# Performance work log

Hardware: AMD Instinct MI355X
Metric: run time of the kernel (lower is better)

Reference implementation:

```python
import jax, jax.numpy as jnp
import numpy as np

B = 8192
N = 2048  # output_dim; input_dim = 4*N


def setup_inputs() -> dict:
    key = jax.random.key(0)
    k1, k2, k3, k4, k5 = jax.random.split(key, 5)
    weight = jax.random.normal(k1, (B, 4 * N), dtype=jnp.float32)
    fc_w = jax.random.normal(k2, (N, 4 * N), dtype=jnp.float32) * 0.02
    fc_b = jax.random.normal(k3, (N,), dtype=jnp.float32) * 0.02
    # per-sample coin flips (torch.rand(1) < 0.5), precomputed as constants
    swap1 = jax.random.randint(k4, (B,), 0, 2, dtype=jnp.int32)
    swap2 = jax.random.randint(k5, (B,), 0, 2, dtype=jnp.int32)
    return {"weight": weight, "fc_w": fc_w, "fc_b": fc_b, "swap1": swap1, "swap2": swap2}


def _permute_rows(x, swap1, swap2):
    # x: [B, 4, n]. Sequential swaps: first swap rows (1,2) if swap1, then
    # swap rows (2,3) (of the already-swapped tensor) if swap2.
    s1 = swap1.astype(bool)
    s2 = swap2.astype(bool)
    r0 = jnp.zeros_like(swap1)
    r1 = jnp.where(s1, 2, 1)
    mid = jnp.where(s1, 1, 2)  # what sits at row 2 after swap1
    r2 = jnp.where(s2, 3, mid)
    r3 = jnp.where(s2, mid, 3)
    perm = jnp.stack([r0, r1, r2, r3], axis=1)  # [B, 4]
    return jnp.take_along_axis(x, perm[:, :, None], axis=1)


def reference(weight, fc_w, fc_b, swap1, swap2):
    b = weight.shape[0]
    n = fc_w.shape[0]
    x = weight.reshape(b, 4, n)
    x = _permute_rows(x, swap1, swap2)
    x = x.reshape(b, 4 * n)
    return x @ fc_w.T + fc_b
```

## Files before the change

kernel.cpp:

```cpp
#include <hip/hip_runtime.h>
#include <hip/hip_bf16.h>
#include <stdint.h>


using f32x4   = __attribute__((ext_vector_type(4))) float;
using bf16x8  = __attribute__((ext_vector_type(8))) __bf16;
using ushort8 = __attribute__((ext_vector_type(8))) unsigned short;

#define B_ROWS 8192
#define K_TOT  8192
#define N_OUT  2048
#define BK     64
#define NT     (K_TOT / BK)

__device__ __forceinline__ unsigned short f2bf(float f) {
  union { float f; unsigned int u; } v;
  v.f = f;
  unsigned int r = v.u + 0x7FFFu + ((v.u >> 16) & 1u);
  return (unsigned short)(r >> 16);
}

__device__ __forceinline__ int perm_src(int r, int s1, int s2) {
  int mid = s1 ? 1 : 2;
  return (r == 0) ? 0
       : (r == 1) ? (s1 ? 2 : 1)
       : (r == 2) ? (s2 ? 3 : mid)
                  : (s2 ? mid : 3);
}

__global__ __launch_bounds__(256) void k_permute_convert(
    const float* __restrict__ w, const int* __restrict__ s1v,
    const int* __restrict__ s2v, unsigned short* __restrict__ xbf) {
  const int blk = blockIdx.x;
  const int b = blk >> 2, r = blk & 3;
  const int s1 = s1v[b] != 0, s2 = s2v[b] != 0;
  const int pr = perm_src(r, s1, s2);
  const float* src = w + (size_t)b * K_TOT + (size_t)pr * 2048 + threadIdx.x * 8;
  unsigned short* dst = xbf + (size_t)b * K_TOT + (size_t)r * 2048 + threadIdx.x * 8;
  f32x4 v0 = *(const f32x4*)src;
  f32x4 v1 = *(const f32x4*)(src + 4);
  ushort8 o;
#pragma unroll
  for (int j = 0; j < 4; ++j) o[j] = f2bf(v0[j]);
#pragma unroll
  for (int j = 0; j < 4; ++j) o[4 + j] = f2bf(v1[j]);
  *(ushort8*)dst = o;
}

__global__ __launch_bounds__(256) void k_convert_w(
    const float* __restrict__ fw, unsigned short* __restrict__ wbf) {
  const size_t base = ((size_t)blockIdx.x * 256 + threadIdx.x) * 8;
  f32x4 v0 = *(const f32x4*)(fw + base);
  f32x4 v1 = *(const f32x4*)(fw + base + 4);
  ushort8 o;
#pragma unroll
  for (int j = 0; j < 4; ++j) o[j] = f2bf(v0[j]);
#pragma unroll
  for (int j = 0; j < 4; ++j) o[4 + j] = f2bf(v1[j]);
  *(ushort8*)(wbf + base) = o;
}

__device__ __forceinline__ void gload16(const unsigned short* g,
                                        const unsigned short* l) {
  __builtin_amdgcn_global_load_lds(
      (__attribute__((address_space(1))) void*)(uintptr_t)(const void*)g,
      (__attribute__((address_space(3))) void*)(unsigned int)(uintptr_t)(const void*)l,
      16, 0, 0);
}


#define VMW4 asm volatile("s_waitcnt vmcnt(4)" ::: "memory")
#define VMW0 asm volatile("s_waitcnt vmcnt(0)" ::: "memory")
#define VMWN ((void)0)
#define LGKM0_FENCE do { \
    asm volatile("s_waitcnt lgkmcnt(0)" ::: "memory"); \
    __builtin_amdgcn_sched_barrier(0); } while (0)

#define LDA(BU, MH, M, KKI) \
  (*(const bf16x8*)(smb + (BU)*65536 + aBase + ((MH)*64 + (M)*16)*128 + colsw[KKI]))
#define LDB(BU, NH, N, KKI) \
  (*(const bf16x8*)(smb + (BU)*65536 + 32768 + bBase + ((NH)*32 + (N)*16)*128 + colsw[KKI]))

#define STAGE(BU, OPL, GOP, H, T) do { \
  gload16((GOP) + (size_t)((H)*128 + row0) * K_TOT + (size_t)(T)*BK + sl0, \
          smu + (BU)*32768 + (OPL) + (H)*8192 + tid*8); \
  gload16((GOP) + (size_t)((H)*128 + row1) * K_TOT + (size_t)(T)*BK + sl1, \
          smu + (BU)*32768 + (OPL) + (H)*8192 + 4096 + tid*8); \
} while (0)

#define QUAD(MH, NH, B0A, B1A) do { \
  _Pragma("unroll") for (int m_ = 0; m_ < 4; ++m_) \
    _Pragma("unroll") for (int n_ = 0; n_ < 2; ++n_) { \
      acc[(MH)*4+m_][(NH)*2+n_] = __builtin_amdgcn_mfma_f32_16x16x32_bf16( \
          aR0[m_], B0A[n_], acc[(MH)*4+m_][(NH)*2+n_], 0, 0, 0); \
      acc[(MH)*4+m_][(NH)*2+n_] = __builtin_amdgcn_mfma_f32_16x16x32_bf16( \
          aR1[m_], B1A[n_], acc[(MH)*4+m_][(NH)*2+n_], 0, 0, 0); \
    } \
} while (0)

#define TILE(BU, T, DOA, DOB, WAIT) do { \
  _Pragma("unroll") for (int m_ = 0; m_ < 4; ++m_) { \
    aR0[m_] = LDA(BU, 0, m_, 0); aR1[m_] = LDA(BU, 0, m_, 1); } \
  _Pragma("unroll") for (int n_ = 0; n_ < 2; ++n_) { \
    bL0[n_] = LDB(BU, 0, n_, 0); bL1[n_] = LDB(BU, 0, n_, 1); } \
  if (DOA) STAGE((BU) ^ 1, 0, gA, 0, (T) + 1); \
  __builtin_amdgcn_s_barrier(); \
  LGKM0_FENCE; \
  __builtin_amdgcn_s_setprio(1); QUAD(0, 0, bL0, bL1); __builtin_amdgcn_s_setprio(0); \
  __builtin_amdgcn_s_barrier(); \
  _Pragma("unroll") for (int n_ = 0; n_ < 2; ++n_) { \
    bH0[n_] = LDB(BU, 1, n_, 0); bH1[n_] = LDB(BU, 1, n_, 1); } \
  if (DOA) STAGE((BU) ^ 1, 0, gA, 1, (T) + 1); \
  __builtin_amdgcn_s_barrier(); \
  LGKM0_FENCE; \
  __builtin_amdgcn_s_setprio(1); QUAD(0, 1, bH0, bH1); __builtin_amdgcn_s_setprio(0); \
  __builtin_amdgcn_s_barrier(); \
  _Pragma("unroll") for (int m_ = 0; m_ < 4; ++m_) { \
    aR0[m_] = LDA(BU, 1, m_, 0); aR1[m_] = LDA(BU, 1, m_, 1); } \
  if (DOB) STAGE(BU, 16384, gB, 0, (T) + 2); \
  __builtin_amdgcn_s_barrier(); \
  LGKM0_FENCE; \
  __builtin_amdgcn_s_setprio(1); QUAD(1, 0, bL0, bL1); __builtin_amdgcn_s_setprio(0); \
  __builtin_amdgcn_s_barrier(); \
  if (DOB) STAGE(BU, 16384, gB, 1, (T) + 2); \
  __builtin_amdgcn_s_barrier(); \
  __builtin_amdgcn_s_setprio(1); QUAD(1, 1, bH0, bH1); __builtin_amdgcn_s_setprio(0); \
  WAIT; \
  __builtin_amdgcn_s_barrier(); \
} while (0)

__global__ __launch_bounds__(512, 2) void k_gemm8(
    const unsigned short* __restrict__ A,
    const unsigned short* __restrict__ Bw,
    const float* __restrict__ bias,
    float* __restrict__ C) {
  __shared__ unsigned short sm[2 * 32768];
  unsigned short* smu = sm;
  const char* smb = (const char*)sm;

  const int tid  = threadIdx.x;
  const int lane = tid & 63;
  const int wave = tid >> 6;
  const int wr = wave >> 2;
  const int wc = wave & 3;
  const int bn = blockIdx.x & 7;
  const int bm = blockIdx.x >> 3;

  const unsigned short* gA = A  + (size_t)bm * 256 * K_TOT;
  const unsigned short* gB = Bw + (size_t)bn * 256 * K_TOT;

  const int row0 = tid >> 3;
  const int sl0  = (((tid & 7) ^ (row0 & 7)) << 3);
  const int row1 = (512 + tid) >> 3;
  const int sl1  = ((((512 + tid) & 7) ^ (row1 & 7)) << 3);

  const int l15 = lane & 15;
  int colsw[2];
  colsw[0] = (((lane >> 4) << 4)) ^ ((lane & 7) << 4);
  colsw[1] = (64 | ((lane >> 4) << 4)) ^ ((lane & 7) << 4);
  const int aBase = (wr * 128 + l15) * 128;
  const int bBase = (wc * 64 + l15) * 128;

  f32x4 acc[8][4];
#pragma unroll
  for (int i = 0; i < 8; ++i)
#pragma unroll
    for (int j = 0; j < 4; ++j) {
      acc[i][j][0] = 0.f; acc[i][j][1] = 0.f; acc[i][j][2] = 0.f; acc[i][j][3] = 0.f;
    }
  bf16x8 aR0[4], aR1[4], bL0[2], bL1[2], bH0[2], bH1[2];

  STAGE(0, 0,     gA, 0, 0);
  STAGE(0, 0,     gA, 1, 0);
  STAGE(0, 16384, gB, 0, 0);
  STAGE(0, 16384, gB, 1, 0);
  STAGE(1, 16384, gB, 0, 1);
  STAGE(1, 16384, gB, 1, 1);
  VMW4;
  __builtin_amdgcn_s_barrier();

  int t = 0;
  for (; t < NT - 4; t += 2) {
    TILE(0, t,     true, true, VMW4);
    TILE(1, t + 1, true, true, VMW4);
  }
  TILE(0, 124, true,  true,  VMW4);
  TILE(1, 125, true,  true,  VMW4);
  TILE(0, 126, true,  false, VMW0);
  TILE(1, 127, false, false, VMWN);

  const int crow0 = bm * 256 + wr * 128 + ((lane >> 4) << 2);
  const int ccol0 = bn * 256 + wc * 64 + l15;
  float bv[4];
#pragma unroll
  for (int n = 0; n < 4; ++n) bv[n] = bias[ccol0 + n * 16];
#pragma unroll
  for (int mi = 0; mi < 8; ++mi)
#pragma unroll
    for (int ni = 0; ni < 4; ++ni) {
      const int r = crow0 + mi * 16;
      const int c = ccol0 + ni * 16;
#pragma unroll
      for (int j = 0; j < 4; ++j)
        C[(size_t)(r + j) * N_OUT + c] = acc[mi][ni][j] + bv[ni];
    }
}

__global__ __launch_bounds__(256) void k_gemm_fallback(
    const float* __restrict__ W, const float* __restrict__ FW,
    const float* __restrict__ bias, const int* __restrict__ s1v,
    const int* __restrict__ s2v, float* __restrict__ C) {
  __shared__ float As[64][33];
  __shared__ float Bs[64][33];
  const int tid = threadIdx.x;
  const int tx = tid & 15, ty = tid >> 4;
  const int bm = blockIdx.x & 127;
  const int bn = blockIdx.x >> 7;
  float acc[4][4] = {{0.f}};
  for (int k0 = 0; k0 < K_TOT; k0 += 32) {
#pragma unroll
    for (int i = 0; i < 8; ++i) {
      int idx = i * 256 + tid;
      int rr = idx >> 5, cc = idx & 31;
      int grow = bm * 64 + rr;
      int gk = k0 + cc;
      int blkr = gk >> 11, within = gk & 2047;
      int s1 = s1v[grow] != 0, s2 = s2v[grow] != 0;
      int pr = perm_src(blkr, s1, s2);
      As[rr][cc] = W[(size_t)grow * K_TOT + (size_t)pr * 2048 + within];
      Bs[rr][cc] = FW[(size_t)(bn * 64 + rr) * K_TOT + gk];
    }
    __syncthreads();
#pragma unroll 8
    for (int kk = 0; kk < 32; ++kk) {
      float a[4], b[4];
#pragma unroll
      for (int i = 0; i < 4; ++i) a[i] = As[ty * 4 + i][kk];
#pragma unroll
      for (int j = 0; j < 4; ++j) b[j] = Bs[tx * 4 + j][kk];
#pragma unroll
      for (int i = 0; i < 4; ++i)
#pragma unroll
        for (int j = 0; j < 4; ++j) acc[i][j] += a[i] * b[j];
    }
    __syncthreads();
  }
#pragma unroll
  for (int i = 0; i < 4; ++i)
#pragma unroll
    for (int j = 0; j < 4; ++j) {
      int r = bm * 64 + ty * 4 + i, c = bn * 64 + tx * 4 + j;
      C[(size_t)r * N_OUT + c] = acc[i][j] + bias[c];
    }
}

extern "C" void kernel_launch(void* const* d_in, const int* in_sizes, int n_in,
                              void* d_out, int out_size, void* d_ws, size_t ws_size,
                              hipStream_t stream) {
  const float* weight = (const float*)d_in[0];
  const float* fc_w   = (const float*)d_in[1];
  const float* fc_b   = (const float*)d_in[2];
  const int*   swap1  = (const int*)d_in[3];
  const int*   swap2  = (const int*)d_in[4];
  float* out = (float*)d_out;

  const size_t xbf_bytes = (size_t)B_ROWS * K_TOT * 2;
  const size_t wbf_bytes = (size_t)N_OUT * K_TOT * 2;
  if (ws_size >= xbf_bytes + wbf_bytes) {
    unsigned short* xbf = (unsigned short*)d_ws;
    unsigned short* wbf = (unsigned short*)((char*)d_ws + xbf_bytes);
    k_permute_convert<<<B_ROWS * 4, 256, 0, stream>>>(weight, swap1, swap2, xbf);
    k_convert_w<<<(N_OUT * K_TOT) / 2048, 256, 0, stream>>>(fc_w, wbf);
    k_gemm8<<<32 * 8, 512, 0, stream>>>(xbf, wbf, fc_b, out);
  } else {
    k_gemm_fallback<<<128 * 32, 256, 0, stream>>>(weight, fc_w, fc_b, swap1,
                                                  swap2, out);
  }
}
```

Measured before the change: 295.7 us.

## Load B operand directly from global into registers and merge prep kernels

The GEMM now keeps only the A tile in LDS and loads the B (weight) fragments straight from global memory into registers, prefetching the next k-step. This halves the shared-memory footprint and drops most barriers per tile. The two fp32-to-bf16 prep kernels are merged into one launch to save a launch and a tail. The cost is that B reads bypass LDS reuse: each wave fetches its own B fragments from global/L2 with less coalesced access, and every tile now ends with a full vmcnt(0) wait.

Result: slower. 474.0 us (+60.3%).

```diff
diff --git a/kernel.cpp b/kernel.cpp
--- a/kernel.cpp
+++ b/kernel.cpp
@@ -28,15 +28,24 @@
                   : (s2 ? mid : 3);
 }
 
-__global__ __launch_bounds__(256) void k_permute_convert(
+__global__ __launch_bounds__(256) void k_prep(
     const float* __restrict__ w, const int* __restrict__ s1v,
-    const int* __restrict__ s2v, unsigned short* __restrict__ xbf) {
+    const int* __restrict__ s2v, const float* __restrict__ fw,
+    unsigned short* __restrict__ xbf, unsigned short* __restrict__ wbf) {
   const int blk = blockIdx.x;
-  const int b = blk >> 2, r = blk & 3;
-  const int s1 = s1v[b] != 0, s2 = s2v[b] != 0;
-  const int pr = perm_src(r, s1, s2);
-  const float* src = w + (size_t)b * K_TOT + (size_t)pr * 2048 + threadIdx.x * 8;
-  unsigned short* dst = xbf + (size_t)b * K_TOT + (size_t)r * 2048 + threadIdx.x * 8;
+  const float* src;
+  unsigned short* dst;
+  if (blk < B_ROWS * 4) {
+    const int b = blk >> 2, r = blk & 3;
+    const int s1 = s1v[b] != 0, s2 = s2v[b] != 0;
+    const int pr = perm_src(r, s1, s2);
+    src = w + (size_t)b * K_TOT + (size_t)pr * 2048 + threadIdx.x * 8;
+    dst = xbf + (size_t)b * K_TOT + (size_t)r * 2048 + threadIdx.x * 8;
+  } else {
+    const size_t base = ((size_t)(blk - B_ROWS * 4) * 256 + threadIdx.x) * 8;
+    src = fw + base;
+    dst = wbf + base;
+  }
   f32x4 v0 = *(const f32x4*)src;
   f32x4 v1 = *(const f32x4*)(src + 4);
   ushort8 o;
@@ -45,19 +54,6 @@
 #pragma unroll
   for (int j = 0; j < 4; ++j) o[4 + j] = f2bf(v1[j]);
   *(ushort8*)dst = o;
-}
-
-__global__ __launch_bounds__(256) void k_convert_w(
-    const float* __restrict__ fw, unsigned short* __restrict__ wbf) {
-  const size_t base = ((size_t)blockIdx.x * 256 + threadIdx.x) * 8;
-  f32x4 v0 = *(const f32x4*)(fw + base);
-  f32x4 v1 = *(const f32x4*)(fw + base + 4);
-  ushort8 o;
-#pragma unroll
-  for (int j = 0; j < 4; ++j) o[j] = f2bf(v0[j]);
-#pragma unroll
-  for (int j = 0; j < 4; ++j) o[4 + j] = f2bf(v1[j]);
-  *(ushort8*)(wbf + base) = o;
 }
 
 __device__ __forceinline__ void gload16(const unsigned short* g,
@@ -68,73 +64,53 @@
       16, 0, 0);
 }
 
-
-#define VMW4 asm volatile("s_waitcnt vmcnt(4)" ::: "memory")
 #define VMW0 asm volatile("s_waitcnt vmcnt(0)" ::: "memory")
-#define VMWN ((void)0)
 #define LGKM0_FENCE do { \
     asm volatile("s_waitcnt lgkmcnt(0)" ::: "memory"); \
     __builtin_amdgcn_sched_barrier(0); } while (0)
 
-#define LDA(BU, MH, M, KKI) \
-  (*(const bf16x8*)(smb + (BU)*65536 + aBase + ((MH)*64 + (M)*16)*128 + colsw[KKI]))
-#define LDB(BU, NH, N, KKI) \
-  (*(const bf16x8*)(smb + (BU)*65536 + 32768 + bBase + ((NH)*32 + (N)*16)*128 + colsw[KKI]))
-
-#define STAGE(BU, OPL, GOP, H, T) do { \
-  gload16((GOP) + (size_t)((H)*128 + row0) * K_TOT + (size_t)(T)*BK + sl0, \
-          smu + (BU)*32768 + (OPL) + (H)*8192 + tid*8); \
-  gload16((GOP) + (size_t)((H)*128 + row1) * K_TOT + (size_t)(T)*BK + sl1, \
-          smu + (BU)*32768 + (OPL) + (H)*8192 + 4096 + tid*8); \
-} while (0)
-
-#define QUAD(MH, NH, B0A, B1A) do { \
-  _Pragma("unroll") for (int m_ = 0; m_ < 4; ++m_) \
-    _Pragma("unroll") for (int n_ = 0; n_ < 2; ++n_) { \
-      acc[(MH)*4+m_][(NH)*2+n_] = __builtin_amdgcn_mfma_f32_16x16x32_bf16( \
-          aR0[m_], B0A[n_], acc[(MH)*4+m_][(NH)*2+n_], 0, 0, 0); \
-      acc[(MH)*4+m_][(NH)*2+n_] = __builtin_amdgcn_mfma_f32_16x16x32_bf16( \
-          aR1[m_], B1A[n_], acc[(MH)*4+m_][(NH)*2+n_], 0, 0, 0); \
-    } \
-} while (0)
-
-#define TILE(BU, T, DOA, DOB, WAIT) do { \
-  _Pragma("unroll") for (int m_ = 0; m_ < 4; ++m_) { \
-    aR0[m_] = LDA(BU, 0, m_, 0); aR1[m_] = LDA(BU, 0, m_, 1); } \
-  _Pragma("unroll") for (int n_ = 0; n_ < 2; ++n_) { \
-    bL0[n_] = LDB(BU, 0, n_, 0); bL1[n_] = LDB(BU, 0, n_, 1); } \
-  if (DOA) STAGE((BU) ^ 1, 0, gA, 0, (T) + 1); \
+#define ALD(BUF, KK) do { \
+  _Pragma("unroll") for (int m_ = 0; m_ < 8; ++m_) \
+    ar[m_] = *(const bf16x8*)(smb + (BUF)*32768 + m_*2048 + aCol[KK]); \
+} while (0)
+
+#define BLD(DST, T, KKH) do { \
+  _Pragma("unroll") for (int n_ = 0; n_ < 4; ++n_) \
+    DST[n_] = *(const bf16x8*)(gBb + (boff0 + n_*262144 + (KKH)*64 + (unsigned)(T)*128)); \
+} while (0)
+
+#define APF(BUF, T) do { \
+  _Pragma("unroll") for (int r_ = 0; r_ < 4; ++r_) \
+    gload16(pa0 + (size_t)r_*524288 + (size_t)(T)*64, \
+            smu + (BUF)*16384 + r_*4096 + tid*8); \
+} while (0)
+
+#define MM(BSET) do { \
+  _Pragma("unroll") for (int m_ = 0; m_ < 8; ++m_) \
+    _Pragma("unroll") for (int n_ = 0; n_ < 4; ++n_) \
+      acc[m_][n_] = __builtin_amdgcn_mfma_f32_16x16x32_bf16( \
+          ar[m_], BSET[n_], acc[m_][n_], 0, 0, 0); \
+} while (0)
+
+#define TILE(BUF, T, BK0C, BK0P, DOPF) do { \
+  ALD(BUF, 0); \
+  BLD(bk1, T, 1);                     \
+  if (DOPF) { BLD(BK0P, (T) + 1, 0); APF((BUF) ^ 1, (T) + 1); } \
+  LGKM0_FENCE; \
+  __builtin_amdgcn_s_setprio(1); MM(BK0C); __builtin_amdgcn_s_setprio(0); \
+  ALD(BUF, 1); \
+  LGKM0_FENCE; \
+  __builtin_amdgcn_s_setprio(1); MM(bk1); __builtin_amdgcn_s_setprio(0); \
+  VMW0; \
   __builtin_amdgcn_s_barrier(); \
-  LGKM0_FENCE; \
-  __builtin_amdgcn_s_setprio(1); QUAD(0, 0, bL0, bL1); __builtin_amdgcn_s_setprio(0); \
-  __builtin_amdgcn_s_barrier(); \
-  _Pragma("unroll") for (int n_ = 0; n_ < 2; ++n_) { \
-    bH0[n_] = LDB(BU, 1, n_, 0); bH1[n_] = LDB(BU, 1, n_, 1); } \
-  if (DOA) STAGE((BU) ^ 1, 0, gA, 1, (T) + 1); \
-  __builtin_amdgcn_s_barrier(); \
-  LGKM0_FENCE; \
-  __builtin_amdgcn_s_setprio(1); QUAD(0, 1, bH0, bH1); __builtin_amdgcn_s_setprio(0); \
-  __builtin_amdgcn_s_barrier(); \
-  _Pragma("unroll") for (int m_ = 0; m_ < 4; ++m_) { \
-    aR0[m_] = LDA(BU, 1, m_, 0); aR1[m_] = LDA(BU, 1, m_, 1); } \
-  if (DOB) STAGE(BU, 16384, gB, 0, (T) + 2); \
-  __builtin_amdgcn_s_barrier(); \
-  LGKM0_FENCE; \
-  __builtin_amdgcn_s_setprio(1); QUAD(1, 0, bL0, bL1); __builtin_amdgcn_s_setprio(0); \
-  __builtin_amdgcn_s_barrier(); \
-  if (DOB) STAGE(BU, 16384, gB, 1, (T) + 2); \
-  __builtin_amdgcn_s_barrier(); \
-  __builtin_amdgcn_s_setprio(1); QUAD(1, 1, bH0, bH1); __builtin_amdgcn_s_setprio(0); \
-  WAIT; \
-  __builtin_amdgcn_s_barrier(); \
-} while (0)
-
-__global__ __launch_bounds__(512, 2) void k_gemm8(
+} while (0)
+
+__global__ __launch_bounds__(512, 2) void k_gemm9(
     const unsigned short* __restrict__ A,
     const unsigned short* __restrict__ Bw,
     const float* __restrict__ bias,
     float* __restrict__ C) {
-  __shared__ unsigned short sm[2 * 32768];
+  __shared__ unsigned short sm[2 * 16384];
   unsigned short* smu = sm;
   const char* smb = (const char*)sm;
 
@@ -145,21 +121,23 @@
   const int wc = wave & 3;
   const int bn = blockIdx.x & 7;
   const int bm = blockIdx.x >> 3;
-
-  const unsigned short* gA = A  + (size_t)bm * 256 * K_TOT;
-  const unsigned short* gB = Bw + (size_t)bn * 256 * K_TOT;
-
-  const int row0 = tid >> 3;
-  const int sl0  = (((tid & 7) ^ (row0 & 7)) << 3);
-  const int row1 = (512 + tid) >> 3;
-  const int sl1  = ((((512 + tid) & 7) ^ (row1 & 7)) << 3);
-
   const int l15 = lane & 15;
-  int colsw[2];
-  colsw[0] = (((lane >> 4) << 4)) ^ ((lane & 7) << 4);
-  colsw[1] = (64 | ((lane >> 4) << 4)) ^ ((lane & 7) << 4);
-  const int aBase = (wr * 128 + l15) * 128;
-  const int bBase = (wc * 64 + l15) * 128;
+
+  const unsigned short* gA = A + (size_t)bm * 256 * K_TOT;
+  const char* gBb = (const char*)(Bw + (size_t)bn * 256 * K_TOT);
+
+  const unsigned short* pa0 =
+      gA + (size_t)(tid >> 3) * K_TOT + (size_t)(((tid & 7) ^ ((tid >> 3) & 7)) * 8);
+
+  int aCol[2];
+  {
+    const int rowb = (wr * 128 + l15) * 128;
+    aCol[0] = rowb + ((((lane >> 4) << 4)) ^ ((lane & 7) << 4));
+    aCol[1] = rowb + ((64 | ((lane >> 4) << 4)) ^ ((lane & 7) << 4));
+  }
+
+  const unsigned int boff0 =
+      (unsigned int)((wc * 64 + l15) * (K_TOT * 2) + ((lane >> 4) << 4));
 
   f32x4 acc[8][4];
 #pragma unroll
@@ -168,26 +146,21 @@
     for (int j = 0; j < 4; ++j) {
       acc[i][j][0] = 0.f; acc[i][j][1] = 0.f; acc[i][j][2] = 0.f; acc[i][j][3] = 0.f;
     }
-  bf16x8 aR0[4], aR1[4], bL0[2], bL1[2], bH0[2], bH1[2];
-
-  STAGE(0, 0,     gA, 0, 0);
-  STAGE(0, 0,     gA, 1, 0);
-  STAGE(0, 16384, gB, 0, 0);
-  STAGE(0, 16384, gB, 1, 0);
-  STAGE(1, 16384, gB, 0, 1);
-  STAGE(1, 16384, gB, 1, 1);
-  VMW4;
+  bf16x8 ar[8], bk0a[4], bk0b[4], bk1[4];
+
+  APF(0, 0);
+  BLD(bk0a, 0, 0);
+  VMW0;
   __builtin_amdgcn_s_barrier();
 
-  int t = 0;
-  for (; t < NT - 4; t += 2) {
-    TILE(0, t,     true, true, VMW4);
-    TILE(1, t + 1, true, true, VMW4);
-  }
-  TILE(0, 124, true,  true,  VMW4);
-  TILE(1, 125, true,  true,  VMW4);
-  TILE(0, 126, true,  false, VMW0);
-  TILE(1, 127, false, false, VMWN);
+  for (int t = 0; t < NT - 4; t += 2) {
+    TILE(0, t,     bk0a, bk0b, true);
+    TILE(1, t + 1, bk0b, bk0a, true);
+  }
+  TILE(0, 124, bk0a, bk0b, true);
+  TILE(1, 125, bk0b, bk0a, true);
+  TILE(0, 126, bk0a, bk0b, true);
+  TILE(1, 127, bk0b, bk0a, false);
 
   const int crow0 = bm * 256 + wr * 128 + ((lane >> 4) << 2);
   const int ccol0 = bn * 256 + wc * 64 + l15;
@@ -269,9 +242,9 @@
   if (ws_size >= xbf_bytes + wbf_bytes) {
     unsigned short* xbf = (unsigned short*)d_ws;
     unsigned short* wbf = (unsigned short*)((char*)d_ws + xbf_bytes);
-    k_permute_convert<<<B_ROWS * 4, 256, 0, stream>>>(weight, swap1, swap2, xbf);
-    k_convert_w<<<(N_OUT * K_TOT) / 2048, 256, 0, stream>>>(fc_w, wbf);
-    k_gemm8<<<32 * 8, 512, 0, stream>>>(xbf, wbf, fc_b, out);
+    k_prep<<<B_ROWS * 4 + (N_OUT * K_TOT) / 2048, 256, 0, stream>>>(
+        weight, swap1, swap2, fc_w, xbf, wbf);
+    k_gemm9<<<32 * 8, 512, 0, stream>>>(xbf, wbf, fc_b, out);
   } else {
     k_gemm_fallback<<<128 * 32, 256, 0, stream>>>(weight, fc_w, fc_b, swap1,
                                                   swap2, out);
```

## Fuse row permutation and bf16 conversion of activations into the GEMM A-loader

Applied to the files above, without the earlier changes.

Removes the separate permute/convert kernel and its bf16 activation workspace. The GEMM now reads fp32 activation rows directly through register loads. Each row's source chunk is picked from packed permutation bits, and the values are converted to bf16 and written into swizzled LDS. Only the weight matrix is still pre-converted and streamed with direct-to-LDS loads. This saves a full read and write pass over the activations. In exchange, the GEMM reads fp32 A, twice as many bytes, once per N-tile, and adds register pressure plus VALU conversion work inside the main loop.

After: 381.5 us. 1.29x slower.

```diff
diff --git a/kernel.cpp b/kernel.cpp
--- a/kernel.cpp
+++ b/kernel.cpp
@@ -18,6 +18,14 @@
   v.f = f;
   unsigned int r = v.u + 0x7FFFu + ((v.u >> 16) & 1u);
   return (unsigned short)(r >> 16);
+}
+
+__device__ __forceinline__ int perm_pack(int s1, int s2) {
+  int mid = s1 ? 1 : 2;
+  int r1 = s1 ? 2 : 1;
+  int r2 = s2 ? 3 : mid;
+  int r3 = s2 ? mid : 3;
+  return (r1 << 2) | (r2 << 4) | (r3 << 6);
 }
 
 __device__ __forceinline__ int perm_src(int r, int s1, int s2) {
@@ -28,26 +36,7 @@
                   : (s2 ? mid : 3);
 }
 
-__global__ __launch_bounds__(256) void k_permute_convert(
-    const float* __restrict__ w, const int* __restrict__ s1v,
-    const int* __restrict__ s2v, unsigned short* __restrict__ xbf) {
-  const int blk = blockIdx.x;
-  const int b = blk >> 2, r = blk & 3;
-  const int s1 = s1v[b] != 0, s2 = s2v[b] != 0;
-  const int pr = perm_src(r, s1, s2);
-  const float* src = w + (size_t)b * K_TOT + (size_t)pr * 2048 + threadIdx.x * 8;
-  unsigned short* dst = xbf + (size_t)b * K_TOT + (size_t)r * 2048 + threadIdx.x * 8;
-  f32x4 v0 = *(const f32x4*)src;
-  f32x4 v1 = *(const f32x4*)(src + 4);
-  ushort8 o;
-#pragma unroll
-  for (int j = 0; j < 4; ++j) o[j] = f2bf(v0[j]);
-#pragma unroll
-  for (int j = 0; j < 4; ++j) o[4 + j] = f2bf(v1[j]);
-  *(ushort8*)dst = o;
-}
-
-__global__ __launch_bounds__(256) void k_convert_w(
+__global__ __launch_bounds__(256) void k_prep_w(
     const float* __restrict__ fw, unsigned short* __restrict__ wbf) {
   const size_t base = ((size_t)blockIdx.x * 256 + threadIdx.x) * 8;
   f32x4 v0 = *(const f32x4*)(fw + base);
@@ -68,10 +57,9 @@
       16, 0, 0);
 }
 
-
-#define VMW4 asm volatile("s_waitcnt vmcnt(4)" ::: "memory")
-#define VMW0 asm volatile("s_waitcnt vmcnt(0)" ::: "memory")
-#define VMWN ((void)0)
+#define VM0 asm volatile("s_waitcnt vmcnt(0)" ::: "memory")
+#define VM2 asm volatile("s_waitcnt vmcnt(2)" ::: "memory")
+#define NOW ((void)0)
 #define LGKM0_FENCE do { \
     asm volatile("s_waitcnt lgkmcnt(0)" ::: "memory"); \
     __builtin_amdgcn_sched_barrier(0); } while (0)
@@ -81,11 +69,34 @@
 #define LDB(BU, NH, N, KKI) \
   (*(const bf16x8*)(smb + (BU)*65536 + 32768 + bBase + ((NH)*32 + (N)*16)*128 + colsw[KKI]))
 
-#define STAGE(BU, OPL, GOP, H, T) do { \
-  gload16((GOP) + (size_t)((H)*128 + row0) * K_TOT + (size_t)(T)*BK + sl0, \
-          smu + (BU)*32768 + (OPL) + (H)*8192 + tid*8); \
-  gload16((GOP) + (size_t)((H)*128 + row1) * K_TOT + (size_t)(T)*BK + sl1, \
-          smu + (BU)*32768 + (OPL) + (H)*8192 + 4096 + tid*8); \
+#define ALD(BUF, MH) do { \
+  _Pragma("unroll") for (int m_ = 0; m_ < 4; ++m_) { \
+    aR0[m_] = LDA(BUF, MH, m_, 0); aR1[m_] = LDA(BUF, MH, m_, 1); } \
+} while (0)
+
+#define STAGEB(BUF, H, T) do { \
+  gload16(gB + (size_t)((H)*128 + row0) * K_TOT + (size_t)(T)*BK + sl0, \
+          smu + (BUF)*32768 + 16384 + (H)*8192 + tid*8); \
+  gload16(gB + (size_t)((H)*128 + row1) * K_TOT + (size_t)(T)*BK + sl0, \
+          smu + (BUF)*32768 + 16384 + (H)*8192 + 4096 + tid*8); \
+} while (0)
+
+#define AOFF(PK, TK) \
+  ((size_t)((((PK) >> ((((TK) >> 5)) << 1)) & 3) << 11) + (size_t)(((TK) & 31) << 6))
+#define ARL0(TK) do { const float* p_ = pA0 + AOFF(PA0, TK); \
+  a0f[0] = *(const f32x4*)p_;        a0f[1] = *(const f32x4*)(p_ + 4); \
+  a0f[2] = *(const f32x4*)(p_ + 8);  a0f[3] = *(const f32x4*)(p_ + 12); } while (0)
+#define ARL1(TK) do { const float* p_ = pA1 + AOFF(PA1, TK); \
+  a1f[0] = *(const f32x4*)p_;        a1f[1] = *(const f32x4*)(p_ + 4); \
+  a1f[2] = *(const f32x4*)(p_ + 8);  a1f[3] = *(const f32x4*)(p_ + 12); } while (0)
+
+#define AWR(BUF, H, AF) do { \
+  bf16x8 lo_, hi_; \
+  _Pragma("unroll") for (int j_ = 0; j_ < 4; ++j_) { \
+    lo_[j_]     = (__bf16)AF[0][j_]; lo_[4 + j_] = (__bf16)AF[1][j_]; \
+    hi_[j_]     = (__bf16)AF[2][j_]; hi_[4 + j_] = (__bf16)AF[3][j_]; } \
+  char* d_ = smw + (BUF)*65536 + ((H)*128 + arow) * 128; \
+  *(bf16x8*)(d_ + wb0) = lo_; *(bf16x8*)(d_ + wb1) = hi_; \
 } while (0)
 
 #define QUAD(MH, NH, B0A, B1A) do { \
@@ -98,45 +109,48 @@
     } \
 } while (0)
 
-#define TILE(BU, T, DOA, DOB, WAIT) do { \
-  _Pragma("unroll") for (int m_ = 0; m_ < 4; ++m_) { \
-    aR0[m_] = LDA(BU, 0, m_, 0); aR1[m_] = LDA(BU, 0, m_, 1); } \
+#define TILE_F(BUF, T, DOA, DOB, WA0, WA1) do { \
+  ALD(BUF, 0); \
   _Pragma("unroll") for (int n_ = 0; n_ < 2; ++n_) { \
-    bL0[n_] = LDB(BU, 0, n_, 0); bL1[n_] = LDB(BU, 0, n_, 1); } \
-  if (DOA) STAGE((BU) ^ 1, 0, gA, 0, (T) + 1); \
+    bL0[n_] = LDB(BUF, 0, n_, 0); bL1[n_] = LDB(BUF, 0, n_, 1); } \
+  if (DOA) ARL0((T) + 1); \
   __builtin_amdgcn_s_barrier(); \
   LGKM0_FENCE; \
   __builtin_amdgcn_s_setprio(1); QUAD(0, 0, bL0, bL1); __builtin_amdgcn_s_setprio(0); \
   __builtin_amdgcn_s_barrier(); \
   _Pragma("unroll") for (int n_ = 0; n_ < 2; ++n_) { \
-    bH0[n_] = LDB(BU, 1, n_, 0); bH1[n_] = LDB(BU, 1, n_, 1); } \
-  if (DOA) STAGE((BU) ^ 1, 0, gA, 1, (T) + 1); \
+    bH0[n_] = LDB(BUF, 1, n_, 0); bH1[n_] = LDB(BUF, 1, n_, 1); } \
   __builtin_amdgcn_s_barrier(); \
   LGKM0_FENCE; \
   __builtin_amdgcn_s_setprio(1); QUAD(0, 1, bH0, bH1); __builtin_amdgcn_s_setprio(0); \
   __builtin_amdgcn_s_barrier(); \
-  _Pragma("unroll") for (int m_ = 0; m_ < 4; ++m_) { \
-    aR0[m_] = LDA(BU, 1, m_, 0); aR1[m_] = LDA(BU, 1, m_, 1); } \
-  if (DOB) STAGE(BU, 16384, gB, 0, (T) + 2); \
+  ALD(BUF, 1); \
+  if (DOB) STAGEB(BUF, 0, (T) + 2); \
+  WA0; \
+  if (DOA) { AWR((BUF) ^ 1, 0, a0f); ARL1((T) + 1); } \
   __builtin_amdgcn_s_barrier(); \
   LGKM0_FENCE; \
   __builtin_amdgcn_s_setprio(1); QUAD(1, 0, bL0, bL1); __builtin_amdgcn_s_setprio(0); \
   __builtin_amdgcn_s_barrier(); \
-  if (DOB) STAGE(BU, 16384, gB, 1, (T) + 2); \
+  if (DOB) STAGEB(BUF, 1, (T) + 2); \
+  WA1; \
+  if (DOA) AWR((BUF) ^ 1, 1, a1f); \
   __builtin_amdgcn_s_barrier(); \
   __builtin_amdgcn_s_setprio(1); QUAD(1, 1, bH0, bH1); __builtin_amdgcn_s_setprio(0); \
-  WAIT; \
-  __builtin_amdgcn_s_barrier(); \
-} while (0)
-
-__global__ __launch_bounds__(512, 2) void k_gemm8(
-    const unsigned short* __restrict__ A,
+  asm volatile("s_waitcnt lgkmcnt(0)" ::: "memory"); \
+  __builtin_amdgcn_s_barrier(); \
+} while (0)
+
+__global__ __launch_bounds__(512, 2) void k_gemm10(
+    const float* __restrict__ W,
+    const int* __restrict__ s1v, const int* __restrict__ s2v,
     const unsigned short* __restrict__ Bw,
     const float* __restrict__ bias,
     float* __restrict__ C) {
   __shared__ unsigned short sm[2 * 32768];
   unsigned short* smu = sm;
   const char* smb = (const char*)sm;
+  char* smw = (char*)sm;
 
   const int tid  = threadIdx.x;
   const int lane = tid & 63;
@@ -145,16 +159,25 @@
   const int wc = wave & 3;
   const int bn = blockIdx.x & 7;
   const int bm = blockIdx.x >> 3;
-
-  const unsigned short* gA = A  + (size_t)bm * 256 * K_TOT;
+  const int l15 = lane & 15;
+
   const unsigned short* gB = Bw + (size_t)bn * 256 * K_TOT;
 
   const int row0 = tid >> 3;
+  const int row1 = 64 + row0;
   const int sl0  = (((tid & 7) ^ (row0 & 7)) << 3);
-  const int row1 = (512 + tid) >> 3;
-  const int sl1  = ((((512 + tid) & 7) ^ (row1 & 7)) << 3);
-
-  const int l15 = lane & 15;
+
+  const int arow = tid >> 2;
+  const int c16  = (tid & 3) << 4;
+  const int rA0 = bm * 256 + arow;
+  const int rA1 = rA0 + 128;
+  const float* pA0 = W + (size_t)rA0 * K_TOT + c16;
+  const float* pA1 = W + (size_t)rA1 * K_TOT + c16;
+  const int PA0 = perm_pack(s1v[rA0] != 0, s2v[rA0] != 0);
+  const int PA1 = perm_pack(s1v[rA1] != 0, s2v[rA1] != 0);
+  const int wb0 = ((((tid & 3) * 2)    ) ^ (arow & 7)) << 4;
+  const int wb1 = ((((tid & 3) * 2) | 1) ^ (arow & 7)) << 4;
+
   int colsw[2];
   colsw[0] = (((lane >> 4) << 4)) ^ ((lane & 7) << 4);
   colsw[1] = (64 | ((lane >> 4) << 4)) ^ ((lane & 7) << 4);
@@ -169,25 +192,24 @@
       acc[i][j][0] = 0.f; acc[i][j][1] = 0.f; acc[i][j][2] = 0.f; acc[i][j][3] = 0.f;
     }
   bf16x8 aR0[4], aR1[4], bL0[2], bL1[2], bH0[2], bH1[2];
-
-  STAGE(0, 0,     gA, 0, 0);
-  STAGE(0, 0,     gA, 1, 0);
-  STAGE(0, 16384, gB, 0, 0);
-  STAGE(0, 16384, gB, 1, 0);
-  STAGE(1, 16384, gB, 0, 1);
-  STAGE(1, 16384, gB, 1, 1);
-  VMW4;
+  f32x4 a0f[4], a1f[4];
+
+  STAGEB(0, 0, 0); STAGEB(0, 1, 0);
+  STAGEB(1, 0, 1); STAGEB(1, 1, 1);
+  ARL0(0); ARL1(0);
+  VM0;
+  AWR(0, 0, a0f); AWR(0, 1, a1f);
+  LGKM0_FENCE;
   __builtin_amdgcn_s_barrier();
 
-  int t = 0;
-  for (; t < NT - 4; t += 2) {
-    TILE(0, t,     true, true, VMW4);
-    TILE(1, t + 1, true, true, VMW4);
+  for (int t = 0; t < 124; t += 2) {
+    TILE_F(0, t,     true, true, VM2, VM2);
+    TILE_F(1, t + 1, true, true, VM2, VM2);
   }
-  TILE(0, 124, true,  true,  VMW4);
-  TILE(1, 125, true,  true,  VMW4);
-  TILE(0, 126, true,  false, VMW0);
-  TILE(1, 127, false, false, VMWN);
+  TILE_F(0, 124, true,  true,  VM2, VM2);
+  TILE_F(1, 125, true,  true,  VM2, VM2);
+  TILE_F(0, 126, true,  false, VM0, VM0);
+  TILE_F(1, 127, false, false, NOW, NOW);
 
   const int crow0 = bm * 256 + wr * 128 + ((lane >> 4) << 2);
   const int ccol0 = bn * 256 + wc * 64 + l15;
@@ -264,14 +286,11 @@
   const int*   swap2  = (const int*)d_in[4];
   float* out = (float*)d_out;
 
-  const size_t xbf_bytes = (size_t)B_ROWS * K_TOT * 2;
   const size_t wbf_bytes = (size_t)N_OUT * K_TOT * 2;
-  if (ws_size >= xbf_bytes + wbf_bytes) {
-    unsigned short* xbf = (unsigned short*)d_ws;
-    unsigned short* wbf = (unsigned short*)((char*)d_ws + xbf_bytes);
-    k_permute_convert<<<B_ROWS * 4, 256, 0, stream>>>(weight, swap1, swap2, xbf);
-    k_convert_w<<<(N_OUT * K_TOT) / 2048, 256, 0, stream>>>(fc_w, wbf);
-    k_gemm8<<<32 * 8, 512, 0, stream>>>(xbf, wbf, fc_b, out);
+  if (ws_size >= wbf_bytes) {
+    unsigned short* wbf = (unsigned short*)d_ws;
+    k_prep_w<<<(N_OUT * K_TOT) / 2048, 256, 0, stream>>>(fc_w, wbf);
+    k_gemm10<<<32 * 8, 512, 0, stream>>>(weight, swap1, swap2, wbf, fc_b, out);
   } else {
     k_gemm_fallback<<<128 * 32, 256, 0, stream>>>(weight, fc_w, fc_b, swap1,
                                                   swap2, out);
```
